# Kernel tuning notes

Hardware: AMD Instinct MI355X
Metric: run time of the kernel (lower is better)

The kernel has to match this reference:

```python
import jax, jax.numpy as jnp
import numpy as np

DIM = 1280
NUM_HEADS = 16
HEAD_DIM = DIM // NUM_HEADS  # 80
SEQ = 3072


def rotate_half(x):
    half = x.shape[-1] // 2
    return jnp.concatenate([-x[..., half:], x[..., :half]], axis=-1)


def apply_rotary_pos_emb_vision(t, freqs):
    # t: [seq, heads, head_dim]; freqs: [seq, head_dim//2]
    emb = jnp.concatenate([freqs, freqs], axis=-1)  # [seq, head_dim]
    cos = jnp.cos(emb)[:, None, :]
    sin = jnp.sin(emb)[:, None, :]
    return t * cos + rotate_half(t) * sin


def setup_inputs() -> dict:
    key = jax.random.key(0)
    k1, k2, k3, k4, k5 = jax.random.split(key, 5)
    hidden_states = jax.random.normal(k1, (SEQ, DIM), dtype=jnp.float32)
    rotary_pos_emb = jax.random.uniform(k2, (SEQ, HEAD_DIM // 2), dtype=jnp.float32) * 10.0
    cu_seqlens = jnp.arange(5, dtype=jnp.int32) * (SEQ // 4)  # [0,768,1536,2304,3072]
    s = 1.0 / np.sqrt(DIM)
    qkv_w = jax.random.normal(k3, (3 * DIM, DIM), dtype=jnp.float32) * s
    qkv_b = jnp.zeros((3 * DIM,), dtype=jnp.float32)
    proj_w = jax.random.normal(k4, (DIM, DIM), dtype=jnp.float32) * s
    proj_b = jnp.zeros((DIM,), dtype=jnp.float32)
    return {
        "hidden_states": hidden_states,
        "rotary_pos_emb": rotary_pos_emb,
        "cu_seqlens": cu_seqlens,
        "qkv_w": qkv_w,
        "qkv_b": qkv_b,
        "proj_w": proj_w,
        "proj_b": proj_b,
    }


def reference(hidden_states, rotary_pos_emb, cu_seqlens, qkv_w, qkv_b, proj_w, proj_b):
    seq = hidden_states.shape[0]
    qkv = hidden_states @ qkv_w.T + qkv_b  # [seq, 3*dim]
    qkv = qkv.reshape(seq, 3, NUM_HEADS, HEAD_DIM)
    q, k, v = qkv[:, 0], qkv[:, 1], qkv[:, 2]  # each [seq, heads, head_dim]

    q = apply_rotary_pos_emb_vision(q, rotary_pos_emb)
    k = apply_rotary_pos_emb_vision(k, rotary_pos_emb)

    # block-diagonal mask from cu_seqlens: tokens attend only within own segment
    pos = jnp.arange(seq)
    seg = jnp.searchsorted(cu_seqlens[1:], pos, side="right")  # segment id per token
    mask = seg[:, None] == seg[None, :]  # [seq, seq] bool

    # [heads, seq, head_dim]
    qh = q.transpose(1, 0, 2)
    kh = k.transpose(1, 0, 2)
    vh = v.transpose(1, 0, 2)

    scale = 1.0 / np.sqrt(HEAD_DIM)
    scores = jnp.einsum("hqd,hkd->hqk", qh, kh) * scale
    scores = jnp.where(mask[None], scores, jnp.finfo(scores.dtype).min)
    attn = jax.nn.softmax(scores, axis=-1)
    out = jnp.einsum("hqk,hkd->hqd", attn, vh)  # [heads, seq, head_dim]

    out = out.transpose(1, 0, 2).reshape(seq, DIM)
    return out @ proj_w.T + proj_b
```

## Files before the change

### kernel.cpp

```cpp
#include <hip/hip_runtime.h>
#include <cstdint>
#include <cstddef>

#define SEQ 3072
#define DIM 1280
#define NH 16
#define HD 80

typedef __attribute__((ext_vector_type(8))) short s16x8;
typedef __attribute__((ext_vector_type(4))) float f32x4;
typedef unsigned short u16;
typedef unsigned int u32;
typedef unsigned long long u64;

__device__ __forceinline__ u16 f2bf(float f) {
  u32 u = __builtin_bit_cast(u32, f);
  u32 r = (u + 0x7FFFu + ((u >> 16) & 1u)) >> 16;
  return (u16)r;
}
__device__ __forceinline__ float bf2f(u16 b) {
  u32 u = ((u32)b) << 16;
  return __builtin_bit_cast(float, u);
}
__device__ __forceinline__ u32 cvtpk_bf16(float lo, float hi) {
  u32 r;
  asm("v_cvt_pk_bf16_f32 %0, %1, %2" : "=v"(r) : "v"(lo), "v"(hi));
  return r;
}
__device__ __forceinline__ void gload16(const u16* g, u16* lds) {
  __builtin_amdgcn_global_load_lds((const __attribute__((address_space(1))) void*)g,
                                   (__attribute__((address_space(3))) void*)lds,
                                   16, 0, 0);
}

#define N4_A (SEQ*DIM/4)
#define N4_B (3*DIM*DIM/4)
#define N4_C (DIM*DIM/4)
__global__ void cvt_kernel(const float* __restrict__ sa, u16* __restrict__ da,
                           const float* __restrict__ sb, u16* __restrict__ db,
                           const float* __restrict__ sc, u16* __restrict__ dc) {
  int i = blockIdx.x * blockDim.x + threadIdx.x;
  const float* s; u16* d; int j;
  if (i < N4_A)            { s = sa; d = da; j = i; }
  else if (i < N4_A+N4_B)  { s = sb; d = db; j = i - N4_A; }
  else if (i < N4_A+N4_B+N4_C) { s = sc; d = dc; j = i - N4_A - N4_B; }
  else return;
  float4 v = ((const float4*)s)[j];
  ushort4 o;
  o.x = f2bf(v.x); o.y = f2bf(v.y); o.z = f2bf(v.z); o.w = f2bf(v.w);
  ((ushort4*)d)[j] = o;
}

__global__ __launch_bounds__(256)
void gemm_kernel(const u16* __restrict__ A, const u16* __restrict__ B,
                 const float* __restrict__ bias,
                 u16* __restrict__ qws, u16* __restrict__ kws, u16* __restrict__ vT,
                 int M, int N, int K)
{
  constexpr int BM = 128, BN = 128, BK = 32;
  __shared__ __align__(16) u16 As[2][BM*BK];
  __shared__ __align__(16) u16 Bs[2][BN*BK];
  const int m0 = blockIdx.y * BM, n0 = blockIdx.x * BN;
  const int tid = threadIdx.x;
  const int lane = tid & 63, wave = tid >> 6;
  const int wr = wave >> 1, wc = wave & 1;
  const int lr = lane & 15, lg = lane >> 4;

  const int c0 = tid, c1 = 256 + tid;
  const int r0 = c0 >> 2, cc0 = c0 & 3;
  const int r1 = c1 >> 2, cc1 = c1 & 3;
  const int wb0 = (tid & ~63), wb1 = 256 + (tid & ~63);

  f32x4 acc[4][4];
  #pragma unroll
  for (int i = 0; i < 4; ++i)
    #pragma unroll
    for (int j = 0; j < 4; ++j) acc[i][j] = (f32x4)0.0f;

  const int NT = K / BK;

  gload16(A + (size_t)(m0 + r0)*K + cc0*8, &As[0][0] + wb0*8);
  gload16(B + (size_t)(n0 + r0)*K + cc0*8, &Bs[0][0] + wb0*8);
  gload16(A + (size_t)(m0 + r1)*K + cc1*8, &As[0][0] + wb1*8);
  gload16(B + (size_t)(n0 + r1)*K + cc1*8, &Bs[0][0] + wb1*8);
  __syncthreads();

  int cur = 0;
  for (int t = 0; t < NT; ++t) {
    if (t + 1 < NT) {
      const int k0 = (t + 1) * BK;
      const int nxt = cur ^ 1;
      gload16(A + (size_t)(m0 + r0)*K + k0 + cc0*8, &As[nxt][0] + wb0*8);
      gload16(B + (size_t)(n0 + r0)*K + k0 + cc0*8, &Bs[nxt][0] + wb0*8);
      gload16(A + (size_t)(m0 + r1)*K + k0 + cc1*8, &As[nxt][0] + wb1*8);
      gload16(B + (size_t)(n0 + r1)*K + k0 + cc1*8, &Bs[nxt][0] + wb1*8);
    }
    s16x8 af[4], bf[4];
    #pragma unroll
    for (int i = 0; i < 4; ++i) {
      af[i] = *(const s16x8*)&As[cur][(wr*64 + i*16 + lr)*BK + lg*8];
      bf[i] = *(const s16x8*)&Bs[cur][(wc*64 + i*16 + lr)*BK + lg*8];
    }
    #pragma unroll
    for (int mi = 0; mi < 4; ++mi)
      #pragma unroll
      for (int ni = 0; ni < 4; ++ni)
        acc[mi][ni] = __builtin_amdgcn_mfma_f32_16x16x32_bf16(af[mi], bf[ni], acc[mi][ni], 0, 0, 0);
    __syncthreads();
    cur ^= 1;
  }

  #pragma unroll
  for (int ni = 0; ni < 4; ++ni) {
    const int n = n0 + wc*64 + ni*16 + lr;
    const float bv = bias[n];
    const int which = n / DIM;
    const int hd = n - which*DIM;
    const int h = hd / HD;
    const int d = hd - h*HD;
    #pragma unroll
    for (int mi = 0; mi < 4; ++mi) {
      const int mb = m0 + wr*64 + mi*16 + lg*4;
      #pragma unroll
      for (int j = 0; j < 4; ++j) {
        const u16 b = f2bf(acc[mi][ni][j] + bv);
        const int m = mb + j;
        if (which == 0)      qws[((size_t)h*SEQ + m)*HD + d] = b;
        else if (which == 1) kws[((size_t)h*SEQ + m)*HD + d] = b;
        else                 vT [((size_t)h*HD + d)*SEQ + m] = b;
      }
    }
  }
}

__global__ __launch_bounds__(128)
void gemm1_kernel(const u16* __restrict__ A, const u16* __restrict__ B,
                  const float* __restrict__ bias, float* __restrict__ fout,
                  int M, int N, int K)
{
  constexpr int BM = 128, BN = 64, BK = 32;
  __shared__ __align__(16) u16 As[2][BM*BK];
  __shared__ __align__(16) u16 Bs[2][BN*BK];
  const int m0 = blockIdx.y * BM, n0 = blockIdx.x * BN;
  const int tid = threadIdx.x;
  const int lane = tid & 63, wave = tid >> 6;
  const int lr = lane & 15, lg = lane >> 4;

  int rA[4], cA[4], wbA[4];
  #pragma unroll
  for (int i = 0; i < 4; ++i) {
    const int c = i*128 + tid;
    rA[i] = c >> 2; cA[i] = c & 3;
    wbA[i] = i*128 + (tid & ~63);
  }
  int rB[2], cB[2], wbB[2];
  #pragma unroll
  for (int i = 0; i < 2; ++i) {
    const int c = i*128 + tid;
    rB[i] = c >> 2; cB[i] = c & 3;
    wbB[i] = i*128 + (tid & ~63);
  }

  f32x4 acc[4][4];
  #pragma unroll
  for (int i = 0; i < 4; ++i)
    #pragma unroll
    for (int j = 0; j < 4; ++j) acc[i][j] = (f32x4)0.0f;

  const int NT = K / BK;

  auto stage = [&](int t, int buf) {
    const int k0 = t * BK;
    #pragma unroll
    for (int i = 0; i < 4; ++i)
      gload16(A + (size_t)(m0 + rA[i])*K + k0 + cA[i]*8, &As[buf][0] + wbA[i]*8);
    #pragma unroll
    for (int i = 0; i < 2; ++i)
      gload16(B + (size_t)(n0 + rB[i])*K + k0 + cB[i]*8, &Bs[buf][0] + wbB[i]*8);
  };

  stage(0, 0);
  __syncthreads();

  int cur = 0;
  for (int t = 0; t < NT; ++t) {
    if (t + 1 < NT) stage(t + 1, cur ^ 1);
    s16x8 af[4], bf[4];
    #pragma unroll
    for (int i = 0; i < 4; ++i) {
      af[i] = *(const s16x8*)&As[cur][(wave*64 + i*16 + lr)*BK + lg*8];
      bf[i] = *(const s16x8*)&Bs[cur][(i*16 + lr)*BK + lg*8];
    }
    #pragma unroll
    for (int mi = 0; mi < 4; ++mi)
      #pragma unroll
      for (int ni = 0; ni < 4; ++ni)
        acc[mi][ni] = __builtin_amdgcn_mfma_f32_16x16x32_bf16(af[mi], bf[ni], acc[mi][ni], 0, 0, 0);
    __syncthreads();
    cur ^= 1;
  }

  #pragma unroll
  for (int ni = 0; ni < 4; ++ni) {
    const int n = n0 + ni*16 + lr;
    const float bv = bias[n];
    #pragma unroll
    for (int mi = 0; mi < 4; ++mi) {
      const int mb = m0 + wave*64 + mi*16 + lg*4;
      #pragma unroll
      for (int j = 0; j < 4; ++j)
        fout[(size_t)(mb + j)*N + n] = acc[mi][ni][j] + bv;
    }
  }
}

__global__ void rope_tab_kernel(const float* __restrict__ freqs, float2* __restrict__ tab, int n) {
  int i = blockIdx.x*blockDim.x + threadIdx.x;
  if (i >= n) return;
  float f = freqs[i];
  tab[i] = make_float2(cosf(f), sinf(f));
}

__global__ void rope_apply_kernel(u16* __restrict__ q, u16* __restrict__ k,
                                  const float2* __restrict__ tab) {
  int idx = blockIdx.x*blockDim.x + threadIdx.x;
  if (idx >= NH*SEQ*5) return;
  const int c = idx % 5;
  const int s = (idx / 5) % SEQ;
  const int h = idx / (5*SEQ);
  const int d0 = c*8;
  const float2* tp = tab + s*(HD/2) + d0;
  float cs[8], sn[8];
  #pragma unroll
  for (int j = 0; j < 8; ++j) { float2 f = tp[j]; cs[j] = f.x; sn[j] = f.y; }
  const size_t base = ((size_t)h*SEQ + s)*HD;
  {
    s16x8 x = *(const s16x8*)(q + base + d0);
    s16x8 y = *(const s16x8*)(q + base + (HD/2) + d0);
    s16x8 nx, ny;
    #pragma unroll
    for (int j = 0; j < 8; ++j) {
      float xv = bf2f((u16)x[j]), yv = bf2f((u16)y[j]);
      nx[j] = (short)f2bf(xv*cs[j] - yv*sn[j]);
      ny[j] = (short)f2bf(yv*cs[j] + xv*sn[j]);
    }
    *(s16x8*)(q + base + d0) = nx;
    *(s16x8*)(q + base + (HD/2) + d0) = ny;
  }
  {
    s16x8 x = *(const s16x8*)(k + base + d0);
    s16x8 y = *(const s16x8*)(k + base + (HD/2) + d0);
    s16x8 nx, ny;
    #pragma unroll
    for (int j = 0; j < 8; ++j) {
      float xv = bf2f((u16)x[j]), yv = bf2f((u16)y[j]);
      nx[j] = (short)f2bf(xv*cs[j] - yv*sn[j]);
      ny[j] = (short)f2bf(yv*cs[j] + xv*sn[j]);
    }
    *(s16x8*)(k + base + d0) = nx;
    *(s16x8*)(k + base + (HD/2) + d0) = ny;
  }
}

struct AttnState {
  float m_run[2];
  float lp[2];
  f32x4 oacc[2][5];
};

__device__ __forceinline__ void load_kv(const u16* __restrict__ kbase,
                                        const u16* __restrict__ vbase,
                                        int lr, int lg, int kc,
                                        s16x8 (&KF)[2][3], s16x8 (&VF)[5]) {
  int kcl = kc; if (kcl > SEQ-32) kcl = SEQ-32;
  #pragma unroll
  for (int kt = 0; kt < 2; ++kt)
    #pragma unroll
    for (int s = 0; s < 3; ++s) {
      const int d0 = s*32 + lg*8;
      if (d0 < HD) KF[kt][s] = *(const s16x8*)(kbase + (size_t)(kcl + kt*16 + lr)*HD + d0);
      else         KF[kt][s] = (s16x8)(short)0;
    }
  #pragma unroll
  for (int dt = 0; dt < 5; ++dt)
    VF[dt] = *(const s16x8*)(vbase + (size_t)(dt*16 + lr)*SEQ + kcl + lg*8);
}

__device__ __forceinline__ void compute_chunk(int kc, const s16x8 (&KF)[2][3], const s16x8 (&VF)[5],
                                              const s16x8 (&qf)[2][3], AttnState& st,
                                              u16 (&P_lds)[2][16][32],
                                              int lr, int lg, int swz,
                                              int rs0, int re0, int rs1, int re1) {
  const float NEG = -__builtin_inff();
  const float DTH = 8.0f;
  const float kscale = 0.11180339887498949f * 1.44269504088896341f;

  f32x4 sacc[2][2];
  #pragma unroll
  for (int qs = 0; qs < 2; ++qs)
    #pragma unroll
    for (int kt = 0; kt < 2; ++kt) sacc[qs][kt] = (f32x4)0.0f;
  #pragma unroll
  for (int kt = 0; kt < 2; ++kt)
    #pragma unroll
    for (int s = 0; s < 3; ++s) {
      sacc[0][kt] = __builtin_amdgcn_mfma_f32_16x16x32_bf16(KF[kt][s], qf[0][s], sacc[0][kt], 0, 0, 0);
      sacc[1][kt] = __builtin_amdgcn_mfma_f32_16x16x32_bf16(KF[kt][s], qf[1][s], sacc[1][kt], 0, 0, 0);
    }

  float sv[2][8];
  #pragma unroll
  for (int qs = 0; qs < 2; ++qs)
    #pragma unroll
    for (int kt = 0; kt < 2; ++kt)
      #pragma unroll
      for (int j = 0; j < 4; ++j)
        sv[qs][kt*4+j] = sacc[qs][kt][j] * kscale;

  const bool full = __all((kc >= rs0) && (kc+32 <= re0) && (kc >= rs1) && (kc+32 <= re1));
  if (!full) {
    #pragma unroll
    for (int qs = 0; qs < 2; ++qs) {
      const int rsq = qs ? rs1 : rs0, req = qs ? re1 : re0;
      #pragma unroll
      for (int kt = 0; kt < 2; ++kt)
        #pragma unroll
        for (int j = 0; j < 4; ++j) {
          const int key = kc + kt*16 + lg*4 + j;
          if (key < rsq || key >= req) sv[qs][kt*4+j] = NEG;
        }
    }
  }

  float pc[2];
  #pragma unroll
  for (int qs = 0; qs < 2; ++qs) {
    float c = sv[qs][0];
    #pragma unroll
    for (int i = 1; i < 8; ++i) c = fmaxf(c, sv[qs][i]);
    pc[qs] = c;
  }

  const bool nore = __all((pc[0] - st.m_run[0] <= DTH) && (pc[1] - st.m_run[1] <= DTH));
  u32 pk[2][4];
  if (nore) {
    #pragma unroll
    for (int qs = 0; qs < 2; ++qs) {
      const float m = st.m_run[qs];
      float ps = 0.0f;
      #pragma unroll
      for (int i2 = 0; i2 < 4; ++i2) {
        float pa = __builtin_amdgcn_exp2f(sv[qs][2*i2]   - m);
        float pb = __builtin_amdgcn_exp2f(sv[qs][2*i2+1] - m);
        ps += pa + pb;
        pk[qs][i2] = cvtpk_bf16(pa, pb);
      }
      st.lp[qs] += ps;
    }
  } else {
    #pragma unroll
    for (int qs = 0; qs < 2; ++qs) {
      float c = pc[qs];
      c = fmaxf(c, __shfl_xor(c, 16, 64));
      c = fmaxf(c, __shfl_xor(c, 32, 64));
      const float mn = fmaxf(st.m_run[qs], c);
      const float fs = (mn == st.m_run[qs]) ? 1.0f : __builtin_amdgcn_exp2f(st.m_run[qs] - mn);
      float ps = 0.0f;
      #pragma unroll
      for (int i2 = 0; i2 < 4; ++i2) {
        float a0 = sv[qs][2*i2], a1 = sv[qs][2*i2+1];
        float pa = (a0 == NEG) ? 0.0f : __builtin_amdgcn_exp2f(a0 - mn);
        float pb = (a1 == NEG) ? 0.0f : __builtin_amdgcn_exp2f(a1 - mn);
        ps += pa + pb;
        pk[qs][i2] = cvtpk_bf16(pa, pb);
      }
      st.lp[qs] = st.lp[qs] * fs + ps;
      st.m_run[qs] = mn;
      float fr[4];
      #pragma unroll
      for (int j = 0; j < 4; ++j)
        fr[j] = __builtin_bit_cast(float,
                  __builtin_amdgcn_ds_bpermute((lg*4 + j)*4, __builtin_bit_cast(int, fs)));
      #pragma unroll
      for (int dt = 0; dt < 5; ++dt)
        #pragma unroll
        for (int j = 0; j < 4; ++j) st.oacc[qs][dt][j] *= fr[j];
    }
  }

  #pragma unroll
  for (int qs = 0; qs < 2; ++qs) {
    u64 w0 = (u64)pk[qs][0] | ((u64)pk[qs][1] << 32);
    u64 w1 = (u64)pk[qs][2] | ((u64)pk[qs][3] << 32);
    u64* P64 = (u64*)&P_lds[qs][0][0];
    P64[lr*8 + ( lg      ^ (swz<<1))] = w0;
    P64[lr*8 + ((4 + lg) ^ (swz<<1))] = w1;
  }
  s16x8 pa0 = *(const s16x8*)&P_lds[0][lr][(lg ^ swz) * 8];
  s16x8 pa1 = *(const s16x8*)&P_lds[1][lr][(lg ^ swz) * 8];

  #pragma unroll
  for (int dt = 0; dt < 5; ++dt) {
    st.oacc[0][dt] = __builtin_amdgcn_mfma_f32_16x16x32_bf16(pa0, VF[dt], st.oacc[0][dt], 0, 0, 0);
    st.oacc[1][dt] = __builtin_amdgcn_mfma_f32_16x16x32_bf16(pa1, VF[dt], st.oacc[1][dt], 0, 0, 0);
  }
}

__global__ __launch_bounds__(64)
void attn_kernel(const u16* __restrict__ qws, const u16* __restrict__ kws,
                 const u16* __restrict__ vT, const int* __restrict__ cu, int ncu,
                 u16* __restrict__ ows )
{
  __shared__ __align__(16) u16 P_lds[2][16][32];
  const int h = blockIdx.x & 15;
  const int t = blockIdx.x >> 4;
  const int lane = threadIdx.x;
  const int lr = lane & 15, lg = lane >> 4;
  const int q0 = t*32;
  const float NEG = -__builtin_inff();

  int rs0 = cu[0], re0 = cu[1], rs1 = cu[0], re1 = cu[1];
  int ts = cu[0], te = cu[1];
  {
    const int qa = q0 + lr, qb = q0 + 16 + lr;
    for (int i = 1; i < ncu-1; ++i) {
      int lo = cu[i], hi = cu[i+1];
      if (qa    >= lo) { rs0 = lo; re0 = hi; }
      if (qb    >= lo) { rs1 = lo; re1 = hi; }
      if (q0    >= lo) { ts = lo; }
      if (q0+31 >= lo) { te = hi; }
    }
  }

  const u16* kbase = kws + (size_t)h*SEQ*HD;
  const u16* vbase = vT  + (size_t)h*HD*SEQ;

  s16x8 qf[2][3];
  #pragma unroll
  for (int qs = 0; qs < 2; ++qs)
    #pragma unroll
    for (int s = 0; s < 3; ++s) {
      int d0 = s*32 + lg*8;
      if (d0 < HD) qf[qs][s] = *(const s16x8*)(qws + ((size_t)h*SEQ + q0 + qs*16 + lr)*HD + d0);
      else         qf[qs][s] = (s16x8)(short)0;
    }

  AttnState st;
  st.m_run[0] = NEG; st.m_run[1] = NEG;
  st.lp[0] = 0.0f;   st.lp[1] = 0.0f;
  #pragma unroll
  for (int qs = 0; qs < 2; ++qs)
    #pragma unroll
    for (int dt = 0; dt < 5; ++dt) st.oacc[qs][dt] = (f32x4)0.0f;

  const int swz = (lr >> 1) & 3;

  const int kc0 = ts & ~31;
  const int nch = (te - kc0 + 31) >> 5;

  s16x8 kfA[2][3], vfA[5], kfB[2][3], vfB[5];
  load_kv(kbase, vbase, lr, lg, kc0, kfA, vfA);

  int kc = kc0, i = 0;
  for (; i + 2 <= nch; i += 2) {
    load_kv(kbase, vbase, lr, lg, kc+32, kfB, vfB);
    compute_chunk(kc, kfA, vfA, qf, st, P_lds, lr, lg, swz, rs0, re0, rs1, re1);
    load_kv(kbase, vbase, lr, lg, kc+64, kfA, vfA);
    compute_chunk(kc+32, kfB, vfB, qf, st, P_lds, lr, lg, swz, rs0, re0, rs1, re1);
    kc += 64;
  }
  if (i < nch)
    compute_chunk(kc, kfA, vfA, qf, st, P_lds, lr, lg, swz, rs0, re0, rs1, re1);

  #pragma unroll
  for (int qs = 0; qs < 2; ++qs) {
    float l = st.lp[qs];
    l += __shfl_xor(l, 16, 64);
    l += __shfl_xor(l, 32, 64);
    float linv[4];
    #pragma unroll
    for (int j = 0; j < 4; ++j) {
      float lv = __builtin_bit_cast(float,
                   __builtin_amdgcn_ds_bpermute((lg*4 + j)*4, __builtin_bit_cast(int, l)));
      linv[j] = 1.0f / lv;
    }
    #pragma unroll
    for (int dt = 0; dt < 5; ++dt)
      #pragma unroll
      for (int j = 0; j < 4; ++j) {
        float v = st.oacc[qs][dt][j] * linv[j];
        ows[(size_t)(q0 + qs*16 + lg*4 + j)*DIM + h*HD + dt*16 + lr] = f2bf(v);
      }
  }
}

extern "C" void kernel_launch(void* const* d_in, const int* in_sizes, int n_in,
                              void* d_out, int out_size, void* d_ws, size_t ws_size,
                              hipStream_t stream) {
  const float* hidden = (const float*)d_in[0];
  const float* rope   = (const float*)d_in[1];
  const int*   cu     = (const int*)d_in[2];
  const float* qkv_w  = (const float*)d_in[3];
  const float* qkv_b  = (const float*)d_in[4];
  const float* proj_w = (const float*)d_in[5];
  const float* proj_b = (const float*)d_in[6];
  float* out = (float*)d_out;
  const int ncu = in_sizes[2];

  char* ws = (char*)d_ws;
  u16* Abf = (u16*)ws; ws += (size_t)SEQ*DIM*2;
  u16* Wq  = (u16*)ws; ws += (size_t)3*DIM*DIM*2;
  u16* Wp  = (u16*)ws; ws += (size_t)DIM*DIM*2;
  u16* qws = (u16*)ws; ws += (size_t)NH*SEQ*HD*2;
  u16* kws = (u16*)ws; ws += (size_t)NH*SEQ*HD*2;
  u16* vTw = (u16*)ws; ws += (size_t)NH*SEQ*HD*2;
  u16* ows = (u16*)ws; ws += (size_t)SEQ*DIM*2;

  cvt_kernel<<<(N4_A+N4_B+N4_C+255)/256, 256, 0, stream>>>(hidden, Abf, qkv_w, Wq, proj_w, Wp);

  gemm_kernel<<<dim3(3*DIM/128, SEQ/128), 256, 0, stream>>>(
      Abf, Wq, qkv_b, qws, kws, vTw, SEQ, 3*DIM, DIM);

  float2* tab = (float2*)Abf;
  rope_tab_kernel<<<(SEQ*(HD/2) + 255)/256, 256, 0, stream>>>(rope, tab, SEQ*(HD/2));
  rope_apply_kernel<<<(NH*SEQ*5 + 255)/256, 256, 0, stream>>>(qws, kws, tab);

  attn_kernel<<<NH*(SEQ/32), 64, 0, stream>>>(qws, kws, vTw, cu, ncu, ows);

  gemm1_kernel<<<dim3(DIM/64, SEQ/128), 128, 0, stream>>>(
      ows, Wp, proj_b, out, SEQ, DIM, DIM);
}
```

Baseline: 152.0 us.

## Split attention key range across two waves per block with LDS merge

The attention kernel now runs two wavefronts per block. Each wave processes alternating 32-key chunks for the same 32 queries, and the partial softmax states (max, sum, output accumulators) are combined through shared memory before the write-out. This halves the serial chunk loop per wave and adds parallelism within each query tile. The cost is extra LDS, two barriers, and an additional merge step, and the assumption that the stats use a log2-scaled max must match compute_chunk.

```diff
diff --git a/kernel.cpp b/kernel.cpp
--- a/kernel.cpp
+++ b/kernel.cpp
@@ -406,15 +406,20 @@
   }
 }
 
-__global__ __launch_bounds__(64)
+__global__ __launch_bounds__(128)
 void attn_kernel(const u16* __restrict__ qws, const u16* __restrict__ kws,
                  const u16* __restrict__ vT, const int* __restrict__ cu, int ncu,
                  u16* __restrict__ ows )
 {
-  __shared__ __align__(16) u16 P_lds[2][16][32];
+  __shared__ __align__(16) u16 P_lds[2][2][16][32];
+  __shared__ float mstat[2][2][16];
+  __shared__ float lstat[2][2][16];
+  __shared__ float O_lds[32][84];
   const int h = blockIdx.x & 15;
   const int t = blockIdx.x >> 4;
-  const int lane = threadIdx.x;
+  const int tid = threadIdx.x;
+  const int w = tid >> 6;
+  const int lane = tid & 63;
   const int lr = lane & 15, lg = lane >> 4;
   const int q0 = t*32;
   const float NEG = -__builtin_inff();
@@ -457,40 +462,71 @@
 
   const int kc0 = ts & ~31;
   const int nch = (te - kc0 + 31) >> 5;
+  const int n_w = (nch - w + 1) >> 1;
 
   s16x8 kfA[2][3], vfA[5], kfB[2][3], vfB[5];
-  load_kv(kbase, vbase, lr, lg, kc0, kfA, vfA);
-
-  int kc = kc0, i = 0;
-  for (; i + 2 <= nch; i += 2) {
-    load_kv(kbase, vbase, lr, lg, kc+32, kfB, vfB);
-    compute_chunk(kc, kfA, vfA, qf, st, P_lds, lr, lg, swz, rs0, re0, rs1, re1);
-    load_kv(kbase, vbase, lr, lg, kc+64, kfA, vfA);
-    compute_chunk(kc+32, kfB, vfB, qf, st, P_lds, lr, lg, swz, rs0, re0, rs1, re1);
-    kc += 64;
-  }
-  if (i < nch)
-    compute_chunk(kc, kfA, vfA, qf, st, P_lds, lr, lg, swz, rs0, re0, rs1, re1);
+  const int kcw0 = kc0 + w*32;
+  if (n_w > 0) load_kv(kbase, vbase, lr, lg, kcw0, kfA, vfA);
+
+  int kc = kcw0, i = 0;
+  for (; i + 2 <= n_w; i += 2) {
+    load_kv(kbase, vbase, lr, lg, kc+64,  kfB, vfB);
+    compute_chunk(kc, kfA, vfA, qf, st, P_lds[w], lr, lg, swz, rs0, re0, rs1, re1);
+    load_kv(kbase, vbase, lr, lg, kc+128, kfA, vfA);
+    compute_chunk(kc+64, kfB, vfB, qf, st, P_lds[w], lr, lg, swz, rs0, re0, rs1, re1);
+    kc += 128;
+  }
+  if (i < n_w)
+    compute_chunk(kc, kfA, vfA, qf, st, P_lds[w], lr, lg, swz, rs0, re0, rs1, re1);
 
   #pragma unroll
   for (int qs = 0; qs < 2; ++qs) {
-    float l = st.lp[qs];
-    l += __shfl_xor(l, 16, 64);
-    l += __shfl_xor(l, 32, 64);
-    float linv[4];
+    st.lp[qs] += __shfl_xor(st.lp[qs], 16, 64);
+    st.lp[qs] += __shfl_xor(st.lp[qs], 32, 64);
+  }
+  if (lg == 0) {
+    mstat[w][0][lr] = st.m_run[0]; lstat[w][0][lr] = st.lp[0];
+    mstat[w][1][lr] = st.m_run[1]; lstat[w][1][lr] = st.lp[1];
+  }
+  __syncthreads();
+
+  float fac[2][4], lin[2][4];
+  #pragma unroll
+  for (int qs = 0; qs < 2; ++qs)
     #pragma unroll
     for (int j = 0; j < 4; ++j) {
-      float lv = __builtin_bit_cast(float,
-                   __builtin_amdgcn_ds_bpermute((lg*4 + j)*4, __builtin_bit_cast(int, l)));
-      linv[j] = 1.0f / lv;
-    }
-    #pragma unroll
-    for (int dt = 0; dt < 5; ++dt)
-      #pragma unroll
-      for (int j = 0; j < 4; ++j) {
-        float v = st.oacc[qs][dt][j] * linv[j];
-        ows[(size_t)(q0 + qs*16 + lg*4 + j)*DIM + h*HD + dt*16 + lr] = f2bf(v);
-      }
+      const int r = lg*4 + j;
+      const float m0 = mstat[0][qs][r], m1 = mstat[1][qs][r];
+      const float mst = fmaxf(m0, m1);
+      float lst = 0.0f;
+      if (m0 != NEG) lst += lstat[0][qs][r] * __builtin_amdgcn_exp2f(m0 - mst);
+      if (m1 != NEG) lst += lstat[1][qs][r] * __builtin_amdgcn_exp2f(m1 - mst);
+      const float mw = w ? m1 : m0;
+      fac[qs][j] = (mw == NEG) ? 0.0f : __builtin_amdgcn_exp2f(mw - mst);
+      lin[qs][j] = 1.0f / lst;
+    }
+
+  if (w == 1) {
+    #pragma unroll
+    for (int qs = 0; qs < 2; ++qs)
+      #pragma unroll
+      for (int dt = 0; dt < 5; ++dt)
+        #pragma unroll
+        for (int j = 0; j < 4; ++j)
+          O_lds[qs*16 + lg*4 + j][dt*16 + lr] = st.oacc[qs][dt][j] * fac[qs][j];
+  }
+  __syncthreads();
+  if (w == 0) {
+    #pragma unroll
+    for (int qs = 0; qs < 2; ++qs)
+      #pragma unroll
+      for (int dt = 0; dt < 5; ++dt)
+        #pragma unroll
+        for (int j = 0; j < 4; ++j) {
+          float v = (st.oacc[qs][dt][j] * fac[qs][j] + O_lds[qs*16 + lg*4 + j][dt*16 + lr])
+                    * lin[qs][j];
+          ows[(size_t)(q0 + qs*16 + lg*4 + j)*DIM + h*HD + dt*16 + lr] = f2bf(v);
+        }
   }
 }
 
@@ -525,7 +561,7 @@
   rope_tab_kernel<<<(SEQ*(HD/2) + 255)/256, 256, 0, stream>>>(rope, tab, SEQ*(HD/2));
   rope_apply_kernel<<<(NH*SEQ*5 + 255)/256, 256, 0, stream>>>(qws, kws, tab);
 
-  attn_kernel<<<NH*(SEQ/32), 64, 0, stream>>>(qws, kws, vTw, cu, ncu, ows);
+  attn_kernel<<<NH*(SEQ/32), 128, 0, stream>>>(qws, kws, vTw, cu, ncu, ows);
 
   gemm1_kernel<<<dim3(DIM/64, SEQ/128), 128, 0, stream>>>(
       ows, Wp, proj_b, out, SEQ, DIM, DIM);
```

New measurement: 149.8 us. Within noise of the previous version (-1.5%).
